# Kernel optimization log

Hardware: AMD Instinct MI355X
Metric: run time of the kernel (lower is better)

Reference implementation:

```python
import jax, jax.numpy as jnp
import numpy as np

N_NODES = 100000
NEG_SLOPE = 0.01  # F.leaky_relu default


def setup_inputs() -> dict:
    key = jax.random.key(0)
    k1, k2, k3, k4, k5 = jax.random.split(key, 5)
    x = jax.random.normal(k1, (N_NODES, 128), dtype=jnp.float32)
    edge_index = jax.random.randint(k2, (2, 1600000), 0, N_NODES, dtype=jnp.int64)
    # GCNConv linear weights (PyG: x @ W.T), bias added after aggregation
    W1 = jax.random.normal(k3, (128, 128), dtype=jnp.float32) * (1.0 / np.sqrt(128))
    b1 = jnp.zeros((128,), dtype=jnp.float32)
    W2 = jax.random.normal(k4, (128, 128), dtype=jnp.float32) * (1.0 / np.sqrt(128))
    b2 = jnp.zeros((128,), dtype=jnp.float32)
    return {"x": x, "edge_index": edge_index, "W1": W1, "b1": b1, "W2": W2, "b2": b2}


def _gcn_layer(x, W, b, src, dst, norm, self_w):
    # linear transform first (GCNConv order): h = x @ W.T
    h = x @ W.T
    # message passing: sum_j norm_ij * h_j  (edges) + self-loop term h_i / deg_i
    msg = h[src] * norm[:, None]                       # [E, F] gather (memory-bound)
    agg = jax.ops.segment_sum(msg, dst, num_segments=x.shape[0])
    out = agg + h * self_w[:, None] + b
    return out


def reference(x, edge_index, W1, b1, W2, b2):
    src = edge_index[0]
    dst = edge_index[1]
    n = x.shape[0]
    # gcn_norm with self-loops: deg_i = in-degree(dst) + 1
    deg = jax.ops.segment_sum(jnp.ones_like(dst, dtype=x.dtype), dst, num_segments=n) + 1.0
    deg_inv_sqrt = jax.lax.rsqrt(deg)
    norm = deg_inv_sqrt[src] * deg_inv_sqrt[dst]       # edge weights
    self_w = deg_inv_sqrt * deg_inv_sqrt               # self-loop weight = 1/deg

    h = _gcn_layer(x, W1, b1, src, dst, norm, self_w)
    h = jax.nn.leaky_relu(h, NEG_SLOPE)
    # dropout inactive (eval semantics)
    h = _gcn_layer(h, W2, b2, src, dst, norm, self_w)
    h = jax.nn.leaky_relu(h, NEG_SLOPE)
    return h
```

## Files before the change

### kernel.cpp

```cpp
#include <hip/hip_runtime.h>

#define F 128
#define NEG_SLOPE 0.01f
#define NPB 512
#define PMAX 256
#define HB 8192
#define BB 8192
#define CAP 12288

typedef _Float16 half8_t __attribute__((ext_vector_type(8)));
typedef float f32x4 __attribute__((ext_vector_type(4)));


__global__ __launch_bounds__(512) void zero_bcnt(int* __restrict__ bcnt,
                                                 int* __restrict__ bcur) {
    int tid = threadIdx.x;
    if (tid < PMAX) bcnt[tid] = 0;
    else bcur[tid - PMAX] = 0;
}

__global__ __launch_bounds__(256) void hist_kernel(const int* __restrict__ dst,
                                                   int* __restrict__ bcnt,
                                                   int E, int nP,
                                                   const float* __restrict__ W1,
                                                   const float* __restrict__ W2,
                                                   _Float16* __restrict__ W1h,
                                                   _Float16* __restrict__ W2h) {
    __shared__ int h[PMAX];
    int tid = threadIdx.x;
    int hb = gridDim.x - 32;
    if (blockIdx.x >= hb) {
        int i = (blockIdx.x - hb) * 256 + tid;
        const int n4 = F * F / 4;
        const float* in = (i < n4) ? W1 : W2;
        _Float16* out = (i < n4) ? W1h : W2h;
        int j = (i < n4) ? i : i - n4;
        float4 v = ((const float4*)in)[j];
        half8_t hx;
        hx[0] = (_Float16)v.x; hx[1] = (_Float16)v.y;
        hx[2] = (_Float16)v.z; hx[3] = (_Float16)v.w;
        *(int2*)&((_Float16*)out)[j * 4] = *(int2*)&hx;
        return;
    }
    if (tid < PMAX) h[tid] = 0;
    __syncthreads();
    int base = blockIdx.x * HB;
    for (int i = tid; i < HB && base + i < E; i += 256)
        atomicAdd(&h[dst[base + i] >> 9], 1);
    __syncthreads();
    if (tid < nP && h[tid]) atomicAdd(&bcnt[tid], h[tid]);
}

__global__ __launch_bounds__(256) void bin_kernel(const int* __restrict__ src,
                                                  const int* __restrict__ dst,
                                                  const int* __restrict__ bcnt,
                                                  int* __restrict__ bcur,
                                                  int* __restrict__ bbase,
                                                  int* __restrict__ binned,
                                                  int E, int nP) {
    __shared__ int hist[PMAX];
    __shared__ int lbase[PMAX];
    __shared__ int gbase[PMAX];
    __shared__ int cur[PMAX];
    __shared__ int sa[PMAX];
    __shared__ int sb[PMAX];
    __shared__ int buf[BB];
    __shared__ unsigned char b8[BB];
    int tid = threadIdx.x;
    int base = blockIdx.x * BB;
    int myE = E - base; if (myE > BB) myE = BB;

    hist[tid] = 0;
    __syncthreads();
    for (int i = tid; i < myE; i += 256)
        atomicAdd(&hist[dst[base + i] >> 9], 1);
    __syncthreads();
    {
        int v = (tid < nP) ? hist[tid] : 0;
        int run = v;
        sa[tid] = v;
        __syncthreads();
        for (int off = 1; off < PMAX; off <<= 1) {
            int add = (tid >= off) ? sa[tid - off] : 0;
            __syncthreads();
            run += add;
            sa[tid] = run;
            __syncthreads();
        }
        if (tid < nP) { lbase[tid] = run - v; cur[tid] = run - v; }
    }
    {
        int v = (tid < nP) ? bcnt[tid] : 0;
        int run = v;
        sb[tid] = v;
        __syncthreads();
        for (int off = 1; off < PMAX; off <<= 1) {
            int add = (tid >= off) ? sb[tid - off] : 0;
            __syncthreads();
            run += add;
            sb[tid] = run;
            __syncthreads();
        }
        int gexc = run - v;
        if (tid < nP) {
            if (blockIdx.x == 0) bbase[tid] = gexc;
            gbase[tid] = hist[tid] ? gexc + atomicAdd(&bcur[tid], hist[tid]) : 0;
        }
    }
    __syncthreads();
    for (int i = tid; i < myE; i += 256) {
        int d = dst[base + i], s = src[base + i];
        int b = d >> 9;
        int lp = atomicAdd(&cur[b], 1);
        buf[lp] = ((d & (NPB - 1)) << 17) | s;
        b8[lp] = (unsigned char)b;
    }
    __syncthreads();
    for (int j = tid; j < myE; j += 256) {
        int b = b8[j];
        binned[gbase[b] + (j - lbase[b])] = buf[j];
    }
}

__global__ __launch_bounds__(256) void csr_kernel(const int* __restrict__ binned,
                                                  const int* __restrict__ bcnt,
                                                  const int* __restrict__ bbase,
                                                  int* __restrict__ srcs,
                                                  int* __restrict__ offs,
                                                  float* __restrict__ dis, int N) {
    __shared__ int cnt[NPB];
    __shared__ int tmp[NPB];
    __shared__ int cur[NPB];
    __shared__ int buf[CAP];
    int tid = threadIdx.x;
    int b = blockIdx.x;
    int ebase = bbase[b];
    int count = bcnt[b];
    int lo = b << 9;
    cnt[tid] = 0;
    cnt[tid + 256] = 0;
    __syncthreads();
    for (int j = tid; j < count; j += 256)
        atomicAdd(&cnt[binned[ebase + j] >> 17], 1);
    __syncthreads();
    int j0 = tid, j1 = tid + 256;
    int v0 = cnt[j0], v1 = cnt[j1];
    tmp[j0] = v0; tmp[j1] = v1;
    __syncthreads();
    for (int off = 1; off < NPB; off <<= 1) {
        int t0 = tmp[j0] + (j0 >= off ? tmp[j0 - off] : 0);
        int t1 = tmp[j1] + (j1 >= off ? tmp[j1 - off] : 0);
        __syncthreads();
        tmp[j0] = t0; tmp[j1] = t1;
        __syncthreads();
    }
    int e0 = tmp[j0] - v0, e1 = tmp[j1] - v1;
    cur[j0] = e0; cur[j1] = e1;
    int n0 = lo + j0, n1 = lo + j1;
    if (n0 < N) { offs[n0] = ebase + e0; dis[n0] = rsqrtf((float)v0 + 1.0f); }
    if (n1 < N) { offs[n1] = ebase + e1; dis[n1] = rsqrtf((float)v1 + 1.0f); }
    __syncthreads();
    for (int j = tid; j < count; j += 256) {
        int rec = binned[ebase + j];
        int pos = atomicAdd(&cur[rec >> 17], 1);
        int s = rec & 0x1FFFF;
        if (pos < CAP) buf[pos] = s; else srcs[ebase + pos] = s;
    }
    __syncthreads();
    int lim = count < CAP ? count : CAP;
    for (int j = tid; j < lim; j += 256)
        srcs[ebase + j] = buf[j];
}


__device__ __forceinline__ void gemm_core(const half8_t afrag[4],
                                          const _Float16* __restrict__ Wh,
                                          const float* __restrict__ dis,
                                          int tile, int m, int quad,
                                          _Float16* __restrict__ orow) {
    f32x4 acc[8];
#pragma unroll
    for (int t = 0; t < 8; ++t) acc[t] = (f32x4){0.f, 0.f, 0.f, 0.f};
#pragma unroll
    for (int c = 0; c < 4; ++c) {
#pragma unroll
        for (int t = 0; t < 8; ++t) {
            half8_t bfrag = *(const half8_t*)&Wh[(t * 16 + m) * F + c * 32 + quad * 8];
            acc[t] = __builtin_amdgcn_mfma_f32_16x16x32_f16(afrag[c], bfrag, acc[t],
                                                            0, 0, 0);
        }
    }
    float d[4];
#pragma unroll
    for (int r = 0; r < 4; ++r) d[r] = dis[tile * 16 + quad * 4 + r];
#pragma unroll
    for (int t = 0; t < 8; ++t)
#pragma unroll
        for (int r = 0; r < 4; ++r)
            orow[(quad * 4 + r) * F + t * 16 + m] = (_Float16)(acc[t][r] * d[r]);
}

__global__ __launch_bounds__(256) void gemm_a32(const float* __restrict__ A,
                                                const _Float16* __restrict__ Wh,
                                                const float* __restrict__ dis,
                                                _Float16* __restrict__ out,
                                                int ntiles) {
    int wave = threadIdx.x >> 6;
    int lane = threadIdx.x & 63;
    int tile = blockIdx.x * 4 + wave;
    if (tile >= ntiles) return;
    int m = lane & 15, quad = lane >> 4;
    const float* arow = A + (size_t)tile * 16 * F;
    half8_t afrag[4];
#pragma unroll
    for (int c = 0; c < 4; ++c) {
        float4 t0 = *(const float4*)&arow[m * F + c * 32 + quad * 8];
        float4 t1 = *(const float4*)&arow[m * F + c * 32 + quad * 8 + 4];
        afrag[c][0] = (_Float16)t0.x; afrag[c][1] = (_Float16)t0.y;
        afrag[c][2] = (_Float16)t0.z; afrag[c][3] = (_Float16)t0.w;
        afrag[c][4] = (_Float16)t1.x; afrag[c][5] = (_Float16)t1.y;
        afrag[c][6] = (_Float16)t1.z; afrag[c][7] = (_Float16)t1.w;
    }
    gemm_core(afrag, Wh, dis, tile, m, quad, out + (size_t)tile * 16 * F);
}

__global__ __launch_bounds__(256) void gemm_a16(const _Float16* __restrict__ A,
                                                const _Float16* __restrict__ Wh,
                                                const float* __restrict__ dis,
                                                _Float16* __restrict__ out,
                                                int ntiles) {
    int wave = threadIdx.x >> 6;
    int lane = threadIdx.x & 63;
    int tile = blockIdx.x * 4 + wave;
    if (tile >= ntiles) return;
    int m = lane & 15, quad = lane >> 4;
    const _Float16* arow = A + (size_t)tile * 16 * F;
    half8_t afrag[4];
#pragma unroll
    for (int c = 0; c < 4; ++c)
        afrag[c] = *(const half8_t*)&arow[m * F + c * 32 + quad * 8];
    gemm_core(afrag, Wh, dis, tile, m, quad, out + (size_t)tile * 16 * F);
}


#define AGG_BODY(H8)                                                           \
    int node = blockIdx.x * 4 + (threadIdx.x >> 6);                            \
    int lane = threadIdx.x & 63;                                               \
    if (node >= n) return;                                                     \
    int g = lane >> 4;                                                         \
    int fo = lane & 15;                                                        \
    int beg = offs[node];                                                      \
    int end = (node + 1 < n) ? offs[node + 1] : E;                             \
    float di = dis[node];                                                      \
    half8_t hv = H8[(size_t)node * 16 + fo];                                   \
    float4 b0 = ((const float4*)bias)[fo * 2];                                 \
    float4 b1v = ((const float4*)bias)[fo * 2 + 1];                            \
    float acc[8];                                                              \
    _Pragma("unroll") for (int j = 0; j < 8; ++j) acc[j] = 0.f;                \
    if (beg < end) {                                                           \
        int i0 = beg + g, i1 = beg + 4 + g;                                    \
        int s0 = srcs[i0 < end ? i0 : beg];                                    \
        int s1 = srcs[i1 < end ? i1 : beg];                                    \
        float w0 = (i0 < end) ? 1.f : 0.f;                                     \
        float w1 = (i1 < end) ? 1.f : 0.f;                                     \
        for (int e = beg; e < end; e += 8) {                                   \
            int ns0 = s0, ns1 = s1;                                            \
            float nw0 = 0.f, nw1 = 0.f;                                        \
            if (e + 8 < end) {                                                 \
                int j0 = e + 8 + g, j1 = e + 12 + g;                           \
                ns0 = srcs[j0 < end ? j0 : beg];                               \
                ns1 = srcs[j1 < end ? j1 : beg];                               \
                nw0 = (j0 < end) ? 1.f : 0.f;                                  \
                nw1 = (j1 < end) ? 1.f : 0.f;                                  \
            }                                                                  \
            half8_t a0 = H8[(size_t)s0 * 16 + fo];                             \
            half8_t a1 = H8[(size_t)s1 * 16 + fo];                             \
            _Pragma("unroll") for (int j = 0; j < 8; ++j)                      \
                acc[j] += w0 * (float)a0[j] + w1 * (float)a1[j];               \
            s0 = ns0; s1 = ns1; w0 = nw0; w1 = nw1;                            \
        }                                                                      \
    }                                                                          \
    _Pragma("unroll") for (int j = 0; j < 8; ++j) {                            \
        acc[j] += __shfl_xor(acc[j], 16);                                      \
        acc[j] += __shfl_xor(acc[j], 32);                                      \
    }                                                                          \
    if (lane >= 16) return;                                                    \
    acc[0] = di * (acc[0] + (float)hv[0]) + b0.x;                              \
    acc[1] = di * (acc[1] + (float)hv[1]) + b0.y;                              \
    acc[2] = di * (acc[2] + (float)hv[2]) + b0.z;                              \
    acc[3] = di * (acc[3] + (float)hv[3]) + b0.w;                              \
    acc[4] = di * (acc[4] + (float)hv[4]) + b1v.x;                             \
    acc[5] = di * (acc[5] + (float)hv[5]) + b1v.y;                             \
    acc[6] = di * (acc[6] + (float)hv[6]) + b1v.z;                             \
    acc[7] = di * (acc[7] + (float)hv[7]) + b1v.w;                             \
    _Pragma("unroll") for (int j = 0; j < 8; ++j)                              \
        acc[j] = (acc[j] > 0.f) ? acc[j] : acc[j] * NEG_SLOPE;

__global__ __launch_bounds__(256) void agg_to_h(const half8_t* __restrict__ h8,
                                                const float* __restrict__ dis,
                                                const float* __restrict__ bias,
                                                const int* __restrict__ srcs,
                                                const int* __restrict__ offs,
                                                half8_t* __restrict__ out,
                                                int n, int E) {
    AGG_BODY(h8)
    half8_t o;
#pragma unroll
    for (int j = 0; j < 8; ++j) o[j] = (_Float16)acc[j];
    out[(size_t)node * 16 + fo] = o;
}

__global__ __launch_bounds__(256) void agg_to_f(const half8_t* __restrict__ h8,
                                                const float* __restrict__ dis,
                                                const float* __restrict__ bias,
                                                const int* __restrict__ srcs,
                                                const int* __restrict__ offs,
                                                float* __restrict__ out,
                                                int n, int E) {
    AGG_BODY(h8)
    float4 o0 = make_float4(acc[0], acc[1], acc[2], acc[3]);
    float4 o1 = make_float4(acc[4], acc[5], acc[6], acc[7]);
    ((float4*)out)[(size_t)node * 32 + fo * 2] = o0;
    ((float4*)out)[(size_t)node * 32 + fo * 2 + 1] = o1;
}


static inline size_t alup(size_t x) { return (x + 255) & ~(size_t)255; }

extern "C" void kernel_launch(void* const* d_in, const int* in_sizes, int n_in,
                              void* d_out, int out_size, void* d_ws, size_t ws_size,
                              hipStream_t stream) {
    const float* x  = (const float*)d_in[0];
    const int*   ei = (const int*)d_in[1];
    const float* W1 = (const float*)d_in[2];
    const float* b1 = (const float*)d_in[3];
    const float* W2 = (const float*)d_in[4];
    const float* b2 = (const float*)d_in[5];
    float* out = (float*)d_out;

    const int N = in_sizes[0] / F;
    const int E = in_sizes[1] / 2;
    const int* src = ei;
    const int* dst = ei + E;

    char* p = (char*)d_ws;
    int*      bcnt   = (int*)p;      p += alup(PMAX * 4);
    int*      bbase  = (int*)p;      p += alup(PMAX * 4);
    int*      bcur   = (int*)p;      p += alup(PMAX * 4);
    float*    dis    = (float*)p;    p += alup((size_t)N * 4);
    int*      offs   = (int*)p;      p += alup((size_t)N * 4);
    int*      binned = (int*)p;      p += alup((size_t)E * 4);
    int*      srcs   = (int*)p;      p += alup((size_t)E * 4);
    _Float16* g      = (_Float16*)p; p += alup((size_t)N * F * 2);
    _Float16* hh     = (_Float16*)p; p += alup((size_t)N * F * 2);
    _Float16* W1h    = (_Float16*)p; p += alup((size_t)F * F * 2);
    _Float16* W2h    = (_Float16*)p; p += alup((size_t)F * F * 2);

    const int nP = (N + NPB - 1) / NPB;
    const int ntiles = (N + 15) / 16;
    const int gemm_grid = (ntiles + 3) / 4;
    const int agg_grid = (N + 3) / 4;

    zero_bcnt<<<1, 512, 0, stream>>>(bcnt, bcur);
    hist_kernel<<<(E + HB - 1) / HB + 32, 256, 0, stream>>>(dst, bcnt, E, nP,
                                                            W1, W2, W1h, W2h);
    bin_kernel<<<(E + BB - 1) / BB, 256, 0, stream>>>(src, dst, bcnt, bcur,
                                                      bbase, binned, E, nP);
    csr_kernel<<<nP, 256, 0, stream>>>(binned, bcnt, bbase, srcs, offs, dis, N);

    gemm_a32<<<gemm_grid, 256, 0, stream>>>(x, W1h, dis, hh, ntiles);
    agg_to_h<<<agg_grid, 256, 0, stream>>>((const half8_t*)hh, dis, b1, srcs,
                                           offs, (half8_t*)g, N, E);
    gemm_a16<<<gemm_grid, 256, 0, stream>>>(g, W2h, dis, hh, ntiles);
    agg_to_f<<<agg_grid, 256, 0, stream>>>((const half8_t*)hh, dis, b2, srcs,
                                           offs, out, N, E);
}
```

Baseline: 340.3 us.

## Fuse CSR build stages into one cooperative kernel with grid syncs

Replaces the four preprocessing launches (zero, histogram, binning, per-bucket CSR) with one cooperative kernel of 512-thread blocks. A per-block histogram matrix in global memory replaces global atomics, and grid.sync separates the histogram, scatter and CSR phases. Each block computes bucket prefix sums by scanning the histogram matrix. This removes launch gaps and the separate histogram pass over dst, but adds grid-sync cost, a serial loop over all blocks per bucket, and depends on the grid (about 196 blocks here, with large LDS use per block) being co-resident. CAP shrinks to fit the combined shared memory.

```diff
diff --git a/kernel.cpp b/kernel.cpp
--- a/kernel.cpp
+++ b/kernel.cpp
@@ -1,175 +1,161 @@
 #include <hip/hip_runtime.h>
+#include <hip/hip_cooperative_groups.h>
+
+namespace cg = cooperative_groups;
 
 #define F 128
 #define NEG_SLOPE 0.01f
 #define NPB 512
 #define PMAX 256
-#define HB 8192
+#define GMAX 256
 #define BB 8192
-#define CAP 12288
+#define CAP 9216
 
 typedef _Float16 half8_t __attribute__((ext_vector_type(8)));
 typedef float f32x4 __attribute__((ext_vector_type(4)));
 
 
-__global__ __launch_bounds__(512) void zero_bcnt(int* __restrict__ bcnt,
-                                                 int* __restrict__ bcur) {
-    int tid = threadIdx.x;
-    if (tid < PMAX) bcnt[tid] = 0;
-    else bcur[tid - PMAX] = 0;
-}
-
-__global__ __launch_bounds__(256) void hist_kernel(const int* __restrict__ dst,
-                                                   int* __restrict__ bcnt,
-                                                   int E, int nP,
-                                                   const float* __restrict__ W1,
-                                                   const float* __restrict__ W2,
-                                                   _Float16* __restrict__ W1h,
-                                                   _Float16* __restrict__ W2h) {
-    __shared__ int h[PMAX];
-    int tid = threadIdx.x;
-    int hb = gridDim.x - 32;
-    if (blockIdx.x >= hb) {
-        int i = (blockIdx.x - hb) * 256 + tid;
+__global__ __launch_bounds__(512) void csr_coop(const int* __restrict__ src,
+                                                const int* __restrict__ dst,
+                                                int E,
+                                                const float* __restrict__ W1,
+                                                const float* __restrict__ W2,
+                                                _Float16* __restrict__ W1h,
+                                                _Float16* __restrict__ W2h,
+                                                int* __restrict__ hcount,
+                                                int* __restrict__ binned,
+                                                int* __restrict__ srcs,
+                                                int* __restrict__ offs,
+                                                float* __restrict__ dis,
+                                                int N, int nP) {
+    __shared__ int hist[PMAX];
+    __shared__ int lbase[PMAX];
+    __shared__ int gbase[PMAX];
+    __shared__ int curA[PMAX];
+    __shared__ int sa[PMAX];
+    __shared__ int buf2[BB];
+    __shared__ unsigned char b8[BB];
+    __shared__ int cnt[NPB];
+    __shared__ int tmp[NPB];
+    __shared__ int cur2[NPB];
+    __shared__ int bufC[CAP];
+    __shared__ int ebase_s, count_s;
+
+    cg::grid_group grid = cg::this_grid();
+    const int t = threadIdx.x;
+    const int b = blockIdx.x;
+    const int nblk = gridDim.x;
+    const int base = b * BB;
+    int myE = E - base; if (myE > BB) myE = BB; if (myE < 0) myE = 0;
+
+    if (b < 16) {
+        int i = b * 512 + t;
         const int n4 = F * F / 4;
         const float* in = (i < n4) ? W1 : W2;
-        _Float16* out = (i < n4) ? W1h : W2h;
+        _Float16* outw = (i < n4) ? W1h : W2h;
         int j = (i < n4) ? i : i - n4;
         float4 v = ((const float4*)in)[j];
         half8_t hx;
         hx[0] = (_Float16)v.x; hx[1] = (_Float16)v.y;
         hx[2] = (_Float16)v.z; hx[3] = (_Float16)v.w;
-        *(int2*)&((_Float16*)out)[j * 4] = *(int2*)&hx;
-        return;
-    }
-    if (tid < PMAX) h[tid] = 0;
-    __syncthreads();
-    int base = blockIdx.x * HB;
-    for (int i = tid; i < HB && base + i < E; i += 256)
-        atomicAdd(&h[dst[base + i] >> 9], 1);
-    __syncthreads();
-    if (tid < nP && h[tid]) atomicAdd(&bcnt[tid], h[tid]);
-}
-
-__global__ __launch_bounds__(256) void bin_kernel(const int* __restrict__ src,
-                                                  const int* __restrict__ dst,
-                                                  const int* __restrict__ bcnt,
-                                                  int* __restrict__ bcur,
-                                                  int* __restrict__ bbase,
-                                                  int* __restrict__ binned,
-                                                  int E, int nP) {
-    __shared__ int hist[PMAX];
-    __shared__ int lbase[PMAX];
-    __shared__ int gbase[PMAX];
-    __shared__ int cur[PMAX];
-    __shared__ int sa[PMAX];
-    __shared__ int sb[PMAX];
-    __shared__ int buf[BB];
-    __shared__ unsigned char b8[BB];
-    int tid = threadIdx.x;
-    int base = blockIdx.x * BB;
-    int myE = E - base; if (myE > BB) myE = BB;
-
-    hist[tid] = 0;
-    __syncthreads();
-    for (int i = tid; i < myE; i += 256)
+        *(int2*)&((_Float16*)outw)[j * 4] = *(int2*)&hx;
+    }
+    if (t < PMAX) hist[t] = 0;
+    __syncthreads();
+    for (int i = t; i < myE; i += 512)
         atomicAdd(&hist[dst[base + i] >> 9], 1);
     __syncthreads();
-    {
-        int v = (tid < nP) ? hist[tid] : 0;
-        int run = v;
-        sa[tid] = v;
-        __syncthreads();
-        for (int off = 1; off < PMAX; off <<= 1) {
-            int add = (tid >= off) ? sa[tid - off] : 0;
-            __syncthreads();
-            run += add;
-            sa[tid] = run;
-            __syncthreads();
+    if (t < PMAX) hcount[t * GMAX + b] = hist[t];
+    __threadfence();
+    grid.sync();
+
+    int tot_v = 0, pfx_v = 0;
+    if (t < PMAX) {
+        const int* row = hcount + t * GMAX;
+        for (int bl = 0; bl < nblk; ++bl) {
+            int v = row[bl];
+            tot_v += v;
+            pfx_v += (bl < b) ? v : 0;
         }
-        if (tid < nP) { lbase[tid] = run - v; cur[tid] = run - v; }
-    }
-    {
-        int v = (tid < nP) ? bcnt[tid] : 0;
-        int run = v;
-        sb[tid] = v;
-        __syncthreads();
-        for (int off = 1; off < PMAX; off <<= 1) {
-            int add = (tid >= off) ? sb[tid - off] : 0;
-            __syncthreads();
-            run += add;
-            sb[tid] = run;
-            __syncthreads();
-        }
-        int gexc = run - v;
-        if (tid < nP) {
-            if (blockIdx.x == 0) bbase[tid] = gexc;
-            gbase[tid] = hist[tid] ? gexc + atomicAdd(&bcur[tid], hist[tid]) : 0;
-        }
-    }
-    __syncthreads();
-    for (int i = tid; i < myE; i += 256) {
+    }
+    if (t < PMAX) sa[t] = tot_v;
+    __syncthreads();
+    int run = tot_v;
+    for (int off = 1; off < PMAX; off <<= 1) {
+        int add = (t < PMAX && t >= off) ? sa[t - off] : 0;
+        __syncthreads();
+        if (t < PMAX) { run += add; sa[t] = run; }
+        __syncthreads();
+    }
+    int gexc = run - tot_v;
+    if (t < PMAX) gbase[t] = gexc + pfx_v;
+    if (t == b) { ebase_s = gexc; count_s = tot_v; }
+    __syncthreads();
+    int lv = (t < PMAX) ? hist[t] : 0;
+    if (t < PMAX) sa[t] = lv;
+    __syncthreads();
+    int run2 = lv;
+    for (int off = 1; off < PMAX; off <<= 1) {
+        int add = (t < PMAX && t >= off) ? sa[t - off] : 0;
+        __syncthreads();
+        if (t < PMAX) { run2 += add; sa[t] = run2; }
+        __syncthreads();
+    }
+    if (t < PMAX) { lbase[t] = run2 - lv; curA[t] = run2 - lv; }
+    __syncthreads();
+    for (int i = t; i < myE; i += 512) {
         int d = dst[base + i], s = src[base + i];
-        int b = d >> 9;
-        int lp = atomicAdd(&cur[b], 1);
-        buf[lp] = ((d & (NPB - 1)) << 17) | s;
-        b8[lp] = (unsigned char)b;
-    }
-    __syncthreads();
-    for (int j = tid; j < myE; j += 256) {
-        int b = b8[j];
-        binned[gbase[b] + (j - lbase[b])] = buf[j];
-    }
-}
-
-__global__ __launch_bounds__(256) void csr_kernel(const int* __restrict__ binned,
-                                                  const int* __restrict__ bcnt,
-                                                  const int* __restrict__ bbase,
-                                                  int* __restrict__ srcs,
-                                                  int* __restrict__ offs,
-                                                  float* __restrict__ dis, int N) {
-    __shared__ int cnt[NPB];
-    __shared__ int tmp[NPB];
-    __shared__ int cur[NPB];
-    __shared__ int buf[CAP];
-    int tid = threadIdx.x;
-    int b = blockIdx.x;
-    int ebase = bbase[b];
-    int count = bcnt[b];
+        int bk = d >> 9;
+        int lp = atomicAdd(&curA[bk], 1);
+        buf2[lp] = ((d & (NPB - 1)) << 17) | s;
+        b8[lp] = (unsigned char)bk;
+    }
+    __syncthreads();
+    for (int j = t; j < myE; j += 512) {
+        int bk = b8[j];
+        binned[gbase[bk] + (j - lbase[bk])] = buf2[j];
+    }
+    __threadfence();
+    grid.sync();
+
+    if (b >= nP) return;
+    int ebase = ebase_s;
+    int count = count_s;
     int lo = b << 9;
-    cnt[tid] = 0;
-    cnt[tid + 256] = 0;
-    __syncthreads();
-    for (int j = tid; j < count; j += 256)
+    cnt[t] = 0;
+    __syncthreads();
+    for (int j = t; j < count; j += 512)
         atomicAdd(&cnt[binned[ebase + j] >> 17], 1);
     __syncthreads();
-    int j0 = tid, j1 = tid + 256;
-    int v0 = cnt[j0], v1 = cnt[j1];
-    tmp[j0] = v0; tmp[j1] = v1;
+    int v = cnt[t];
+    int run3 = v;
+    tmp[t] = v;
     __syncthreads();
     for (int off = 1; off < NPB; off <<= 1) {
-        int t0 = tmp[j0] + (j0 >= off ? tmp[j0 - off] : 0);
-        int t1 = tmp[j1] + (j1 >= off ? tmp[j1 - off] : 0);
-        __syncthreads();
-        tmp[j0] = t0; tmp[j1] = t1;
-        __syncthreads();
-    }
-    int e0 = tmp[j0] - v0, e1 = tmp[j1] - v1;
-    cur[j0] = e0; cur[j1] = e1;
-    int n0 = lo + j0, n1 = lo + j1;
-    if (n0 < N) { offs[n0] = ebase + e0; dis[n0] = rsqrtf((float)v0 + 1.0f); }
-    if (n1 < N) { offs[n1] = ebase + e1; dis[n1] = rsqrtf((float)v1 + 1.0f); }
-    __syncthreads();
-    for (int j = tid; j < count; j += 256) {
+        int add = (t >= off) ? tmp[t - off] : 0;
+        __syncthreads();
+        run3 += add;
+        tmp[t] = run3;
+        __syncthreads();
+    }
+    int excl = run3 - v;
+    cur2[t] = excl;
+    int node = lo + t;
+    if (node < N) {
+        offs[node] = ebase + excl;
+        dis[node] = rsqrtf((float)v + 1.0f);
+    }
+    __syncthreads();
+    for (int j = t; j < count; j += 512) {
         int rec = binned[ebase + j];
-        int pos = atomicAdd(&cur[rec >> 17], 1);
+        int pos = atomicAdd(&cur2[rec >> 17], 1);
         int s = rec & 0x1FFFF;
-        if (pos < CAP) buf[pos] = s; else srcs[ebase + pos] = s;
+        if (pos < CAP) bufC[pos] = s; else srcs[ebase + pos] = s;
     }
     __syncthreads();
     int lim = count < CAP ? count : CAP;
-    for (int j = tid; j < lim; j += 256)
-        srcs[ebase + j] = buf[j];
+    for (int j = t; j < lim; j += 512)
+        srcs[ebase + j] = bufC[j];
 }
 
 
@@ -180,24 +166,24 @@
                                           _Float16* __restrict__ orow) {
     f32x4 acc[8];
 #pragma unroll
-    for (int t = 0; t < 8; ++t) acc[t] = (f32x4){0.f, 0.f, 0.f, 0.f};
+    for (int tt = 0; tt < 8; ++tt) acc[tt] = (f32x4){0.f, 0.f, 0.f, 0.f};
 #pragma unroll
     for (int c = 0; c < 4; ++c) {
 #pragma unroll
-        for (int t = 0; t < 8; ++t) {
-            half8_t bfrag = *(const half8_t*)&Wh[(t * 16 + m) * F + c * 32 + quad * 8];
-            acc[t] = __builtin_amdgcn_mfma_f32_16x16x32_f16(afrag[c], bfrag, acc[t],
-                                                            0, 0, 0);
+        for (int tt = 0; tt < 8; ++tt) {
+            half8_t bfrag = *(const half8_t*)&Wh[(tt * 16 + m) * F + c * 32 + quad * 8];
+            acc[tt] = __builtin_amdgcn_mfma_f32_16x16x32_f16(afrag[c], bfrag, acc[tt],
+                                                             0, 0, 0);
         }
     }
     float d[4];
 #pragma unroll
     for (int r = 0; r < 4; ++r) d[r] = dis[tile * 16 + quad * 4 + r];
 #pragma unroll
-    for (int t = 0; t < 8; ++t)
+    for (int tt = 0; tt < 8; ++tt)
 #pragma unroll
         for (int r = 0; r < 4; ++r)
-            orow[(quad * 4 + r) * F + t * 16 + m] = (_Float16)(acc[t][r] * d[r]);
+            orow[(quad * 4 + r) * F + tt * 16 + m] = (_Float16)(acc[tt][r] * d[r]);
 }
 
 __global__ __launch_bounds__(256) void gemm_a32(const float* __restrict__ A,
@@ -338,15 +324,13 @@
     const float* b2 = (const float*)d_in[5];
     float* out = (float*)d_out;
 
-    const int N = in_sizes[0] / F;
-    const int E = in_sizes[1] / 2;
+    int N = in_sizes[0] / F;
+    int E = in_sizes[1] / 2;
     const int* src = ei;
     const int* dst = ei + E;
 
     char* p = (char*)d_ws;
-    int*      bcnt   = (int*)p;      p += alup(PMAX * 4);
-    int*      bbase  = (int*)p;      p += alup(PMAX * 4);
-    int*      bcur   = (int*)p;      p += alup(PMAX * 4);
+    int*      hcount = (int*)p;      p += alup((size_t)PMAX * GMAX * 4);
     float*    dis    = (float*)p;    p += alup((size_t)N * 4);
     int*      offs   = (int*)p;      p += alup((size_t)N * 4);
     int*      binned = (int*)p;      p += alup((size_t)E * 4);
@@ -356,17 +340,19 @@
     _Float16* W1h    = (_Float16*)p; p += alup((size_t)F * F * 2);
     _Float16* W2h    = (_Float16*)p; p += alup((size_t)F * F * 2);
 
-    const int nP = (N + NPB - 1) / NPB;
+    int nP  = (N + NPB - 1) / NPB;
+    const int nBB = (E + BB - 1) / BB;
+    int grid = nBB > nP ? nBB : nP;
+    if (grid < 16) grid = 16;
     const int ntiles = (N + 15) / 16;
     const int gemm_grid = (ntiles + 3) / 4;
     const int agg_grid = (N + 3) / 4;
 
-    zero_bcnt<<<1, 512, 0, stream>>>(bcnt, bcur);
-    hist_kernel<<<(E + HB - 1) / HB + 32, 256, 0, stream>>>(dst, bcnt, E, nP,
-                                                            W1, W2, W1h, W2h);
-    bin_kernel<<<(E + BB - 1) / BB, 256, 0, stream>>>(src, dst, bcnt, bcur,
-                                                      bbase, binned, E, nP);
-    csr_kernel<<<nP, 256, 0, stream>>>(binned, bcnt, bbase, srcs, offs, dis, N);
+    void* cargs[] = {(void*)&src, (void*)&dst, (void*)&E,
+                     (void*)&W1, (void*)&W2, (void*)&W1h, (void*)&W2h,
+                     (void*)&hcount, (void*)&binned, (void*)&srcs,
+                     (void*)&offs, (void*)&dis, (void*)&N, (void*)&nP};
+    hipLaunchCooperativeKernel(csr_coop, dim3(grid), dim3(512), cargs, 0, stream);
 
     gemm_a32<<<gemm_grid, 256, 0, stream>>>(x, W1h, dis, hh, ntiles);
     agg_to_h<<<agg_grid, 256, 0, stream>>>((const half8_t*)hh, dis, b1, srcs,
```

Measured after the change: 469.0 us. +37.8%, slower.

## Fuse layer-1 aggregation with layer-2 GEMM through shared memory

Applied to the files above, without the earlier changes.

Merges the first aggregation kernel and the second GEMM into one kernel. Each block aggregates 16 nodes, stages the activated fp16 rows in shared memory, then runs MFMA against W2. This removes one kernel launch and a full N×128 fp16 write and read of the intermediate. The cost is that each wave now handles 4 nodes serially, and the per-block GEMM work adds a barrier, which may reduce latency hiding in the memory-bound gather.

```diff
diff --git a/kernel.cpp b/kernel.cpp
--- a/kernel.cpp
+++ b/kernel.cpp
@@ -173,33 +173,6 @@
 }
 
 
-__device__ __forceinline__ void gemm_core(const half8_t afrag[4],
-                                          const _Float16* __restrict__ Wh,
-                                          const float* __restrict__ dis,
-                                          int tile, int m, int quad,
-                                          _Float16* __restrict__ orow) {
-    f32x4 acc[8];
-#pragma unroll
-    for (int t = 0; t < 8; ++t) acc[t] = (f32x4){0.f, 0.f, 0.f, 0.f};
-#pragma unroll
-    for (int c = 0; c < 4; ++c) {
-#pragma unroll
-        for (int t = 0; t < 8; ++t) {
-            half8_t bfrag = *(const half8_t*)&Wh[(t * 16 + m) * F + c * 32 + quad * 8];
-            acc[t] = __builtin_amdgcn_mfma_f32_16x16x32_f16(afrag[c], bfrag, acc[t],
-                                                            0, 0, 0);
-        }
-    }
-    float d[4];
-#pragma unroll
-    for (int r = 0; r < 4; ++r) d[r] = dis[tile * 16 + quad * 4 + r];
-#pragma unroll
-    for (int t = 0; t < 8; ++t)
-#pragma unroll
-        for (int r = 0; r < 4; ++r)
-            orow[(quad * 4 + r) * F + t * 16 + m] = (_Float16)(acc[t][r] * d[r]);
-}
-
 __global__ __launch_bounds__(256) void gemm_a32(const float* __restrict__ A,
                                                 const _Float16* __restrict__ Wh,
                                                 const float* __restrict__ dis,
@@ -221,25 +194,137 @@
         afrag[c][4] = (_Float16)t1.x; afrag[c][5] = (_Float16)t1.y;
         afrag[c][6] = (_Float16)t1.z; afrag[c][7] = (_Float16)t1.w;
     }
-    gemm_core(afrag, Wh, dis, tile, m, quad, out + (size_t)tile * 16 * F);
-}
-
-__global__ __launch_bounds__(256) void gemm_a16(const _Float16* __restrict__ A,
-                                                const _Float16* __restrict__ Wh,
-                                                const float* __restrict__ dis,
-                                                _Float16* __restrict__ out,
-                                                int ntiles) {
-    int wave = threadIdx.x >> 6;
+    f32x4 acc[8];
+#pragma unroll
+    for (int t = 0; t < 8; ++t) acc[t] = (f32x4){0.f, 0.f, 0.f, 0.f};
+#pragma unroll
+    for (int c = 0; c < 4; ++c) {
+#pragma unroll
+        for (int t = 0; t < 8; ++t) {
+            half8_t bfrag = *(const half8_t*)&Wh[(t * 16 + m) * F + c * 32 + quad * 8];
+            acc[t] = __builtin_amdgcn_mfma_f32_16x16x32_f16(afrag[c], bfrag, acc[t],
+                                                            0, 0, 0);
+        }
+    }
+    float d[4];
+#pragma unroll
+    for (int r = 0; r < 4; ++r) d[r] = dis[tile * 16 + quad * 4 + r];
+    _Float16* orow = out + (size_t)tile * 16 * F;
+#pragma unroll
+    for (int t = 0; t < 8; ++t)
+#pragma unroll
+        for (int r = 0; r < 4; ++r)
+            orow[(quad * 4 + r) * F + t * 16 + m] = (_Float16)(acc[t][r] * d[r]);
+}
+
+
+__global__ __launch_bounds__(256) void agg_gemm16(const half8_t* __restrict__ h8,
+                                                  const float* __restrict__ dis,
+                                                  const float* __restrict__ bias,
+                                                  const _Float16* __restrict__ Wh,
+                                                  const int* __restrict__ srcs,
+                                                  const int* __restrict__ offs,
+                                                  _Float16* __restrict__ out,
+                                                  int n, int E) {
+    __shared__ _Float16 Af[2048];
+    int tile = blockIdx.x;
+    int w = threadIdx.x >> 6;
     int lane = threadIdx.x & 63;
-    int tile = blockIdx.x * 4 + wave;
-    if (tile >= ntiles) return;
-    int m = lane & 15, quad = lane >> 4;
-    const _Float16* arow = A + (size_t)tile * 16 * F;
+    int g = lane >> 4;
+    int fo = lane & 15;
+    float4 b0 = ((const float4*)bias)[fo * 2];
+    float4 b1v = ((const float4*)bias)[fo * 2 + 1];
+
+#pragma unroll
+    for (int i = 0; i < 4; ++i) {
+        int node = tile * 16 + w * 4 + i;
+        int beg = 0, end = 0;
+        if (node < n) {
+            beg = offs[node];
+            end = (node + 1 < n) ? offs[node + 1] : E;
+        }
+        float di = (node < n) ? dis[node] : 0.f;
+        half8_t hv = h8[(size_t)(node < n ? node : 0) * 16 + fo];
+        float acc[8];
+#pragma unroll
+        for (int j = 0; j < 8; ++j) acc[j] = 0.f;
+        if (beg < end) {
+            int i0 = beg + g, i1 = beg + 4 + g;
+            int s0 = srcs[i0 < end ? i0 : beg];
+            int s1 = srcs[i1 < end ? i1 : beg];
+            float w0 = (i0 < end) ? 1.f : 0.f;
+            float w1 = (i1 < end) ? 1.f : 0.f;
+            for (int e = beg; e < end; e += 8) {
+                int ns0 = s0, ns1 = s1;
+                float nw0 = 0.f, nw1 = 0.f;
+                if (e + 8 < end) {
+                    int j0 = e + 8 + g, j1 = e + 12 + g;
+                    ns0 = srcs[j0 < end ? j0 : beg];
+                    ns1 = srcs[j1 < end ? j1 : beg];
+                    nw0 = (j0 < end) ? 1.f : 0.f;
+                    nw1 = (j1 < end) ? 1.f : 0.f;
+                }
+                half8_t a0 = h8[(size_t)s0 * 16 + fo];
+                half8_t a1 = h8[(size_t)s1 * 16 + fo];
+#pragma unroll
+                for (int j = 0; j < 8; ++j)
+                    acc[j] += w0 * (float)a0[j] + w1 * (float)a1[j];
+                s0 = ns0; s1 = ns1; w0 = nw0; w1 = nw1;
+            }
+        }
+#pragma unroll
+        for (int j = 0; j < 8; ++j) {
+            acc[j] += __shfl_xor(acc[j], 16);
+            acc[j] += __shfl_xor(acc[j], 32);
+        }
+        if (lane < 16 && node < n) {
+            acc[0] = di * (acc[0] + (float)hv[0]) + b0.x;
+            acc[1] = di * (acc[1] + (float)hv[1]) + b0.y;
+            acc[2] = di * (acc[2] + (float)hv[2]) + b0.z;
+            acc[3] = di * (acc[3] + (float)hv[3]) + b0.w;
+            acc[4] = di * (acc[4] + (float)hv[4]) + b1v.x;
+            acc[5] = di * (acc[5] + (float)hv[5]) + b1v.y;
+            acc[6] = di * (acc[6] + (float)hv[6]) + b1v.z;
+            acc[7] = di * (acc[7] + (float)hv[7]) + b1v.w;
+            half8_t o;
+#pragma unroll
+            for (int j = 0; j < 8; ++j) {
+                float v = (acc[j] > 0.f) ? acc[j] : acc[j] * NEG_SLOPE;
+                o[j] = (_Float16)v;
+            }
+            *(half8_t*)&Af[(((fo >> 2) * 4 + (fo & 3)) * 16 + (w * 4 + i)) * 8] = o;
+        }
+    }
+    __syncthreads();
+
+    int m = fo, quad = g;
     half8_t afrag[4];
 #pragma unroll
     for (int c = 0; c < 4; ++c)
-        afrag[c] = *(const half8_t*)&arow[m * F + c * 32 + quad * 8];
-    gemm_core(afrag, Wh, dis, tile, m, quad, out + (size_t)tile * 16 * F);
+        afrag[c] = *(const half8_t*)&Af[((c * 4 + quad) * 16 + m) * 8];
+    float d[4];
+#pragma unroll
+    for (int r = 0; r < 4; ++r) {
+        int node = tile * 16 + quad * 4 + r;
+        d[r] = (node < n) ? dis[node] : 0.f;
+    }
+#pragma unroll
+    for (int s = 0; s < 2; ++s) {
+        int t = w * 2 + s;
+        f32x4 acc2 = (f32x4){0.f, 0.f, 0.f, 0.f};
+#pragma unroll
+        for (int c = 0; c < 4; ++c) {
+            half8_t bfrag = *(const half8_t*)&Wh[(t * 16 + m) * F + c * 32 + quad * 8];
+            acc2 = __builtin_amdgcn_mfma_f32_16x16x32_f16(afrag[c], bfrag, acc2,
+                                                          0, 0, 0);
+        }
+#pragma unroll
+        for (int r = 0; r < 4; ++r) {
+            int node = tile * 16 + quad * 4 + r;
+            if (node < n)
+                out[(size_t)node * F + t * 16 + m] = (_Float16)(acc2[r] * d[r]);
+        }
+    }
 }
 
 
@@ -296,20 +381,6 @@
     _Pragma("unroll") for (int j = 0; j < 8; ++j)                              \
         acc[j] = (acc[j] > 0.f) ? acc[j] : acc[j] * NEG_SLOPE;
 
-__global__ __launch_bounds__(256) void agg_to_h(const half8_t* __restrict__ h8,
-                                                const float* __restrict__ dis,
-                                                const float* __restrict__ bias,
-                                                const int* __restrict__ srcs,
-                                                const int* __restrict__ offs,
-                                                half8_t* __restrict__ out,
-                                                int n, int E) {
-    AGG_BODY(h8)
-    half8_t o;
-#pragma unroll
-    for (int j = 0; j < 8; ++j) o[j] = (_Float16)acc[j];
-    out[(size_t)node * 16 + fo] = o;
-}
-
 __global__ __launch_bounds__(256) void agg_to_f(const half8_t* __restrict__ h8,
                                                 const float* __restrict__ dis,
                                                 const float* __restrict__ bias,
@@ -369,9 +440,8 @@
     csr_kernel<<<nP, 256, 0, stream>>>(binned, bcnt, bbase, srcs, offs, dis, N);
 
     gemm_a32<<<gemm_grid, 256, 0, stream>>>(x, W1h, dis, hh, ntiles);
-    agg_to_h<<<agg_grid, 256, 0, stream>>>((const half8_t*)hh, dis, b1, srcs,
-                                           offs, (half8_t*)g, N, E);
-    gemm_a16<<<gemm_grid, 256, 0, stream>>>(g, W2h, dis, hh, ntiles);
-    agg_to_f<<<agg_grid, 256, 0, stream>>>((const half8_t*)hh, dis, b2, srcs,
+    agg_gemm16<<<ntiles, 256, 0, stream>>>((const half8_t*)hh, dis, b1, W2h,
+                                           srcs, offs, g, N, E);
+    agg_to_f<<<agg_grid, 256, 0, stream>>>((const half8_t*)g, dis, b2, srcs,
                                            offs, out, N, E);
 }
```

After: 327.2 us. -3.9%, faster.

## Slice feature tables into 16-column planes for cache-resident aggregation

Applied to the files above, without the earlier changes.

The GEMMs now write their fp16 outputs as eight feature-slice planes, each holding 16 columns for every node, instead of row-major rows. Aggregation launches one block group per slice, with blockIdx low bits selecting the slice. Each pair of lanes gathers one 32-byte half-row per edge, up to 16 edges at a time per node, followed by a shuffle reduction. The goal is to keep each slice's gather working set (about 3.2 MB) in L2/LLC and improve gather locality. In exchange, the edge list is re-read eight times, mostly-idle lanes on low-degree nodes waste work, and the GEMM stores become more strided.

```diff
diff --git a/kernel.cpp b/kernel.cpp
--- a/kernel.cpp
+++ b/kernel.cpp
@@ -173,33 +173,6 @@
 }
 
 
-__device__ __forceinline__ void gemm_core(const half8_t afrag[4],
-                                          const _Float16* __restrict__ Wh,
-                                          const float* __restrict__ dis,
-                                          int tile, int m, int quad,
-                                          _Float16* __restrict__ orow) {
-    f32x4 acc[8];
-#pragma unroll
-    for (int t = 0; t < 8; ++t) acc[t] = (f32x4){0.f, 0.f, 0.f, 0.f};
-#pragma unroll
-    for (int c = 0; c < 4; ++c) {
-#pragma unroll
-        for (int t = 0; t < 8; ++t) {
-            half8_t bfrag = *(const half8_t*)&Wh[(t * 16 + m) * F + c * 32 + quad * 8];
-            acc[t] = __builtin_amdgcn_mfma_f32_16x16x32_f16(afrag[c], bfrag, acc[t],
-                                                            0, 0, 0);
-        }
-    }
-    float d[4];
-#pragma unroll
-    for (int r = 0; r < 4; ++r) d[r] = dis[tile * 16 + quad * 4 + r];
-#pragma unroll
-    for (int t = 0; t < 8; ++t)
-#pragma unroll
-        for (int r = 0; r < 4; ++r)
-            orow[(quad * 4 + r) * F + t * 16 + m] = (_Float16)(acc[t][r] * d[r]);
-}
-
 __global__ __launch_bounds__(256) void gemm_a32(const float* __restrict__ A,
                                                 const _Float16* __restrict__ Wh,
                                                 const float* __restrict__ dis,
@@ -221,8 +194,31 @@
         afrag[c][4] = (_Float16)t1.x; afrag[c][5] = (_Float16)t1.y;
         afrag[c][6] = (_Float16)t1.z; afrag[c][7] = (_Float16)t1.w;
     }
-    gemm_core(afrag, Wh, dis, tile, m, quad, out + (size_t)tile * 16 * F);
-}
+    f32x4 acc[8];
+#pragma unroll
+    for (int t = 0; t < 8; ++t) acc[t] = (f32x4){0.f, 0.f, 0.f, 0.f};
+#pragma unroll
+    for (int c = 0; c < 4; ++c) {
+#pragma unroll
+        for (int t = 0; t < 8; ++t) {
+            half8_t bfrag = *(const half8_t*)&Wh[(t * 16 + m) * F + c * 32 + quad * 8];
+            acc[t] = __builtin_amdgcn_mfma_f32_16x16x32_f16(afrag[c], bfrag, acc[t],
+                                                            0, 0, 0);
+        }
+    }
+    float d[4];
+#pragma unroll
+    for (int r = 0; r < 4; ++r) d[r] = dis[tile * 16 + quad * 4 + r];
+    size_t SL = (size_t)ntiles * 256;
+#pragma unroll
+    for (int t = 0; t < 8; ++t)
+#pragma unroll
+        for (int r = 0; r < 4; ++r) {
+            int node = tile * 16 + quad * 4 + r;
+            out[(size_t)t * SL + (size_t)node * 16 + m] = (_Float16)(acc[t][r] * d[r]);
+        }
+}
+
 
 __global__ __launch_bounds__(256) void gemm_a16(const _Float16* __restrict__ A,
                                                 const _Float16* __restrict__ Wh,
@@ -234,94 +230,109 @@
     int tile = blockIdx.x * 4 + wave;
     if (tile >= ntiles) return;
     int m = lane & 15, quad = lane >> 4;
-    const _Float16* arow = A + (size_t)tile * 16 * F;
+    size_t SL = (size_t)ntiles * 256;
     half8_t afrag[4];
 #pragma unroll
-    for (int c = 0; c < 4; ++c)
-        afrag[c] = *(const half8_t*)&arow[m * F + c * 32 + quad * 8];
-    gemm_core(afrag, Wh, dis, tile, m, quad, out + (size_t)tile * 16 * F);
-}
-
-
-#define AGG_BODY(H8)                                                           \
-    int node = blockIdx.x * 4 + (threadIdx.x >> 6);                            \
+    for (int c = 0; c < 4; ++c) {
+        int fs = c * 2 + (quad >> 1);
+        int off = (quad & 1) * 8;
+        afrag[c] = *(const half8_t*)
+            &A[(size_t)fs * SL + (size_t)(tile * 16 + m) * 16 + off];
+    }
+    f32x4 acc[8];
+#pragma unroll
+    for (int t = 0; t < 8; ++t) acc[t] = (f32x4){0.f, 0.f, 0.f, 0.f};
+#pragma unroll
+    for (int c = 0; c < 4; ++c) {
+#pragma unroll
+        for (int t = 0; t < 8; ++t) {
+            half8_t bfrag = *(const half8_t*)&Wh[(t * 16 + m) * F + c * 32 + quad * 8];
+            acc[t] = __builtin_amdgcn_mfma_f32_16x16x32_f16(afrag[c], bfrag, acc[t],
+                                                            0, 0, 0);
+        }
+    }
+    float d[4];
+#pragma unroll
+    for (int r = 0; r < 4; ++r) d[r] = dis[tile * 16 + quad * 4 + r];
+#pragma unroll
+    for (int t = 0; t < 8; ++t)
+#pragma unroll
+        for (int r = 0; r < 4; ++r) {
+            int node = tile * 16 + quad * 4 + r;
+            out[(size_t)t * SL + (size_t)node * 16 + m] = (_Float16)(acc[t][r] * d[r]);
+        }
+}
+
+
+#define AGS_BODY(TBL)                                                          \
+    int fs = blockIdx.x & 7;                                                   \
+    int ng = blockIdx.x >> 3;                                                  \
+    int w = threadIdx.x >> 6;                                                  \
     int lane = threadIdx.x & 63;                                               \
+    int slot = (lane >> 1) & 15;                                               \
+    int h = lane & 1;                                                          \
+    int node = ng * 8 + w * 2 + (lane >> 5);                                   \
     if (node >= n) return;                                                     \
-    int g = lane >> 4;                                                         \
-    int fo = lane & 15;                                                        \
+    const half8_t* Ts = TBL + (size_t)fs * sl8;                                \
     int beg = offs[node];                                                      \
     int end = (node + 1 < n) ? offs[node + 1] : E;                             \
     float di = dis[node];                                                      \
-    half8_t hv = H8[(size_t)node * 16 + fo];                                   \
-    float4 b0 = ((const float4*)bias)[fo * 2];                                 \
-    float4 b1v = ((const float4*)bias)[fo * 2 + 1];                            \
+    half8_t hv = Ts[(size_t)node * 2 + h];                                     \
+    float4 bb = ((const float4*)bias)[fs * 4 + h * 2];                         \
+    float4 bb2 = ((const float4*)bias)[fs * 4 + h * 2 + 1];                    \
     float acc[8];                                                              \
     _Pragma("unroll") for (int j = 0; j < 8; ++j) acc[j] = 0.f;                \
-    if (beg < end) {                                                           \
-        int i0 = beg + g, i1 = beg + 4 + g;                                    \
-        int s0 = srcs[i0 < end ? i0 : beg];                                    \
-        int s1 = srcs[i1 < end ? i1 : beg];                                    \
-        float w0 = (i0 < end) ? 1.f : 0.f;                                     \
-        float w1 = (i1 < end) ? 1.f : 0.f;                                     \
-        for (int e = beg; e < end; e += 8) {                                   \
-            int ns0 = s0, ns1 = s1;                                            \
-            float nw0 = 0.f, nw1 = 0.f;                                        \
-            if (e + 8 < end) {                                                 \
-                int j0 = e + 8 + g, j1 = e + 12 + g;                           \
-                ns0 = srcs[j0 < end ? j0 : beg];                               \
-                ns1 = srcs[j1 < end ? j1 : beg];                               \
-                nw0 = (j0 < end) ? 1.f : 0.f;                                  \
-                nw1 = (j1 < end) ? 1.f : 0.f;                                  \
-            }                                                                  \
-            half8_t a0 = H8[(size_t)s0 * 16 + fo];                             \
-            half8_t a1 = H8[(size_t)s1 * 16 + fo];                             \
-            _Pragma("unroll") for (int j = 0; j < 8; ++j)                      \
-                acc[j] += w0 * (float)a0[j] + w1 * (float)a1[j];               \
-            s0 = ns0; s1 = ns1; w0 = nw0; w1 = nw1;                            \
-        }                                                                      \
+    for (int e = beg; e < end; e += 16) {                                      \
+        int idx = e + slot;                                                    \
+        int s = __builtin_nontemporal_load(&srcs[idx < end ? idx : beg]);      \
+        float wv = (idx < end) ? 1.f : 0.f;                                    \
+        half8_t a = Ts[(size_t)s * 2 + h];                                     \
+        _Pragma("unroll") for (int j = 0; j < 8; ++j)                          \
+            acc[j] += wv * (float)a[j];                                        \
     }                                                                          \
     _Pragma("unroll") for (int j = 0; j < 8; ++j) {                            \
+        acc[j] += __shfl_xor(acc[j], 2);                                       \
+        acc[j] += __shfl_xor(acc[j], 4);                                       \
+        acc[j] += __shfl_xor(acc[j], 8);                                       \
         acc[j] += __shfl_xor(acc[j], 16);                                      \
-        acc[j] += __shfl_xor(acc[j], 32);                                      \
     }                                                                          \
-    if (lane >= 16) return;                                                    \
-    acc[0] = di * (acc[0] + (float)hv[0]) + b0.x;                              \
-    acc[1] = di * (acc[1] + (float)hv[1]) + b0.y;                              \
-    acc[2] = di * (acc[2] + (float)hv[2]) + b0.z;                              \
-    acc[3] = di * (acc[3] + (float)hv[3]) + b0.w;                              \
-    acc[4] = di * (acc[4] + (float)hv[4]) + b1v.x;                             \
-    acc[5] = di * (acc[5] + (float)hv[5]) + b1v.y;                             \
-    acc[6] = di * (acc[6] + (float)hv[6]) + b1v.z;                             \
-    acc[7] = di * (acc[7] + (float)hv[7]) + b1v.w;                             \
+    if (slot != 0) return;                                                     \
+    acc[0] = di * (acc[0] + (float)hv[0]) + bb.x;                              \
+    acc[1] = di * (acc[1] + (float)hv[1]) + bb.y;                              \
+    acc[2] = di * (acc[2] + (float)hv[2]) + bb.z;                              \
+    acc[3] = di * (acc[3] + (float)hv[3]) + bb.w;                              \
+    acc[4] = di * (acc[4] + (float)hv[4]) + bb2.x;                             \
+    acc[5] = di * (acc[5] + (float)hv[5]) + bb2.y;                             \
+    acc[6] = di * (acc[6] + (float)hv[6]) + bb2.z;                             \
+    acc[7] = di * (acc[7] + (float)hv[7]) + bb2.w;                             \
     _Pragma("unroll") for (int j = 0; j < 8; ++j)                              \
         acc[j] = (acc[j] > 0.f) ? acc[j] : acc[j] * NEG_SLOPE;
 
-__global__ __launch_bounds__(256) void agg_to_h(const half8_t* __restrict__ h8,
-                                                const float* __restrict__ dis,
-                                                const float* __restrict__ bias,
-                                                const int* __restrict__ srcs,
-                                                const int* __restrict__ offs,
-                                                half8_t* __restrict__ out,
-                                                int n, int E) {
-    AGG_BODY(h8)
+__global__ __launch_bounds__(256) void agg_h_slice(const half8_t* __restrict__ tbl,
+                                                   const float* __restrict__ dis,
+                                                   const float* __restrict__ bias,
+                                                   const int* __restrict__ srcs,
+                                                   const int* __restrict__ offs,
+                                                   half8_t* __restrict__ gout,
+                                                   int n, int E, int sl8) {
+    AGS_BODY(tbl)
     half8_t o;
 #pragma unroll
     for (int j = 0; j < 8; ++j) o[j] = (_Float16)acc[j];
-    out[(size_t)node * 16 + fo] = o;
-}
-
-__global__ __launch_bounds__(256) void agg_to_f(const half8_t* __restrict__ h8,
-                                                const float* __restrict__ dis,
-                                                const float* __restrict__ bias,
-                                                const int* __restrict__ srcs,
-                                                const int* __restrict__ offs,
-                                                float* __restrict__ out,
-                                                int n, int E) {
-    AGG_BODY(h8)
-    float4 o0 = make_float4(acc[0], acc[1], acc[2], acc[3]);
-    float4 o1 = make_float4(acc[4], acc[5], acc[6], acc[7]);
-    ((float4*)out)[(size_t)node * 32 + fo * 2] = o0;
-    ((float4*)out)[(size_t)node * 32 + fo * 2 + 1] = o1;
+    gout[(size_t)fs * sl8 + (size_t)node * 2 + h] = o;
+}
+
+__global__ __launch_bounds__(256) void agg_f_slice(const half8_t* __restrict__ tbl,
+                                                   const float* __restrict__ dis,
+                                                   const float* __restrict__ bias,
+                                                   const int* __restrict__ srcs,
+                                                   const int* __restrict__ offs,
+                                                   float* __restrict__ out,
+                                                   int n, int E, int sl8) {
+    AGS_BODY(tbl)
+    float* op = out + (size_t)node * F + fs * 16 + h * 8;
+    *(float4*)op = make_float4(acc[0], acc[1], acc[2], acc[3]);
+    *(float4*)(op + 4) = make_float4(acc[4], acc[5], acc[6], acc[7]);
 }
 
 
@@ -343,6 +354,9 @@
     const int* src = ei;
     const int* dst = ei + E;
 
+    const int ntiles = (N + 15) / 16;
+    const size_t tblsz = (size_t)ntiles * 16 * F * 2;
+
     char* p = (char*)d_ws;
     int*      bcnt   = (int*)p;      p += alup(PMAX * 4);
     int*      bbase  = (int*)p;      p += alup(PMAX * 4);
@@ -351,15 +365,15 @@
     int*      offs   = (int*)p;      p += alup((size_t)N * 4);
     int*      binned = (int*)p;      p += alup((size_t)E * 4);
     int*      srcs   = (int*)p;      p += alup((size_t)E * 4);
-    _Float16* g      = (_Float16*)p; p += alup((size_t)N * F * 2);
-    _Float16* hh     = (_Float16*)p; p += alup((size_t)N * F * 2);
+    _Float16* gS     = (_Float16*)p; p += alup(tblsz);
+    _Float16* hhS    = (_Float16*)p; p += alup(tblsz);
     _Float16* W1h    = (_Float16*)p; p += alup((size_t)F * F * 2);
     _Float16* W2h    = (_Float16*)p; p += alup((size_t)F * F * 2);
 
     const int nP = (N + NPB - 1) / NPB;
-    const int ntiles = (N + 15) / 16;
     const int gemm_grid = (ntiles + 3) / 4;
-    const int agg_grid = (N + 3) / 4;
+    const int agg_grid = ((N + 7) / 8) * 8;
+    const int sl8 = ntiles * 32;
 
     zero_bcnt<<<1, 512, 0, stream>>>(bcnt, bcur);
     hist_kernel<<<(E + HB - 1) / HB + 32, 256, 0, stream>>>(dst, bcnt, E, nP,
@@ -368,10 +382,10 @@
                                                       bbase, binned, E, nP);
     csr_kernel<<<nP, 256, 0, stream>>>(binned, bcnt, bbase, srcs, offs, dis, N);
 
-    gemm_a32<<<gemm_grid, 256, 0, stream>>>(x, W1h, dis, hh, ntiles);
-    agg_to_h<<<agg_grid, 256, 0, stream>>>((const half8_t*)hh, dis, b1, srcs,
-                                           offs, (half8_t*)g, N, E);
-    gemm_a16<<<gemm_grid, 256, 0, stream>>>(g, W2h, dis, hh, ntiles);
-    agg_to_f<<<agg_grid, 256, 0, stream>>>((const half8_t*)hh, dis, b2, srcs,
-                                           offs, out, N, E);
-}
+    gemm_a32<<<gemm_grid, 256, 0, stream>>>(x, W1h, dis, hhS, ntiles);
+    agg_h_slice<<<agg_grid, 256, 0, stream>>>((const half8_t*)hhS, dis, b1,
+                                              srcs, offs, (half8_t*)gS, N, E, sl8);
+    gemm_a16<<<gemm_grid, 256, 0, stream>>>(gS, W2h, dis, hhS, ntiles);
+    agg_f_slice<<<agg_grid, 256, 0, stream>>>((const half8_t*)hhS, dis, b2,
+                                              srcs, offs, out, N, E, sl8);
+}
```

New measurement: 555.0 us. 1.63x slower.
